# Kernel optimization log

Measured on AMD Instinct MI355X. Metric: run time of the kernel, lower is better.

## Reference

```python
import jax, jax.numpy as jnp
import numpy as np

LAMBDA_SOFTMAX = 9.0
LAMBDA_LSE = 6.0
MARGIN = 0.2
EPS = 1e-8


def setup_inputs() -> dict:
    key = jax.random.key(0)
    k1, k2, k3 = jax.random.split(key, 3)
    Ni, R, W, d = 128, 36, 50, 1024
    im = jax.random.normal(k1, (Ni, R, d), dtype=jnp.float32)
    s = jax.random.normal(k2, (Ni, W, d), dtype=jnp.float32)
    s_l = jax.random.randint(k3, (Ni,), 5, W + 1, dtype=jnp.int32)
    return {"im": im, "s": s, "s_l": s_l}


def _scan_t2i_scores(im, s, s_l):
    # im: (Ni, R, d) images; s: (Nc, W, d) captions; s_l: (Nc,) caption lengths
    Nc, W, _ = s.shape
    word_mask = jnp.arange(W)[None, :] < s_l[:, None]          # (Nc, W)
    # attn[c,i,r,w] = <im[i,r], s[c,w]>  (bmm(context, query^T) per caption)
    attn = jnp.einsum('ird,cwd->cirw', im, s)                  # (Nc, Ni, R, W)
    # clipped_l2norm: LeakyReLU(0.1) then l2-normalize over word dim
    attn = jax.nn.leaky_relu(attn, 0.1)
    attn = attn * word_mask[:, None, None, :]                  # zero padded words
    norm = jnp.sqrt(jnp.sum(attn * attn, axis=3, keepdims=True)) + EPS
    attn = attn / norm
    # transpose to (Nc, Ni, W, R), smooth-softmax over regions
    attn_t = jax.nn.softmax(jnp.swapaxes(attn, 2, 3) * LAMBDA_SOFTMAX, axis=-1)
    # weighted image context per word: (Nc, Ni, W, d)
    wei = jnp.einsum('ird,ciwr->ciwd', im, attn_t)
    # cosine similarity along d between cap word and weighted context
    w12 = jnp.einsum('cwd,ciwd->ciw', s, wei)                  # (Nc, Ni, W)
    w1 = jnp.linalg.norm(s, axis=-1)                           # (Nc, W)
    w2 = jnp.linalg.norm(wei, axis=-1)                         # (Nc, Ni, W)
    row_sim = w12 / jnp.clip(w1[:, None, :] * w2, EPS, None)
    # LogSumExp aggregation over valid words only
    e = jnp.where(word_mask[:, None, :], jnp.exp(row_sim * LAMBDA_LSE), 0.0)
    sims = jnp.log(jnp.sum(e, axis=2)) / LAMBDA_LSE            # (Nc, Ni)
    return sims.T                                              # scores[i, c]


def reference(im, s, s_l) -> jnp.ndarray:
    scores = _scan_t2i_scores(im, s, s_l)                      # (Ni, Nc), Ni == Nc
    diag = jnp.diag(scores)[:, None]
    cost_s = jnp.clip(MARGIN + scores - diag, 0.0, None)       # caption retrieval
    cost_im = jnp.clip(MARGIN + scores - diag.T, 0.0, None)    # image retrieval
    eye = jnp.eye(scores.shape[0], dtype=bool)
    cost_s = jnp.where(eye, 0.0, cost_s)
    cost_im = jnp.where(eye, 0.0, cost_im)
    # max_violation=True: hardest negative per row/column
    return jnp.max(cost_s, axis=1).sum() + jnp.max(cost_im, axis=0).sum()
```

## Files before the change

kernel.cpp:

```cpp
#include <hip/hip_runtime.h>
#include <hip/hip_bf16.h>
#include <cstdint>

using u16 = unsigned short;
using u32 = unsigned int;
using bf16x8 = __attribute__((ext_vector_type(8))) short;
using f32x4  = __attribute__((ext_vector_type(4))) float;

#define NI 128
#define NC 128
#define RR 36
#define WW 50
#define DD 1024
#define LDC 6400
#define ATS 37
#define IMN ((size_t)NI * RR * DD)
#define SN  ((size_t)NC * WW * DD)

#define GLL16(g, l) __builtin_amdgcn_global_load_lds(                        \
    (const __attribute__((address_space(1))) void*)(g),                      \
    (__attribute__((address_space(3))) void*)(l), 16, 0, 0)

typedef const __attribute__((address_space(4))) float cfloat;

__device__ __forceinline__ float2 bf16pair(u32 u) {
  float2 f;
  f.x = __uint_as_float(u << 16);
  f.y = __uint_as_float(u & 0xffff0000u);
  return f;
}

__device__ __forceinline__ u32 bf16_rne(u32 x) {
  return (x + 0x7FFFu + ((x >> 16) & 1u)) >> 16;
}

__global__ __launch_bounds__(256) void detect_dtype(const u16* __restrict__ im,
                                                    int* __restrict__ flag) {
  __shared__ int cnt;
  if (threadIdx.x == 0) cnt = 0;
  __syncthreads();
  int local = 0;
#pragma unroll
  for (int v = 0; v < 32; ++v) {
    u16 u = im[threadIdx.x * 32 + v];
    int e = (u >> 7) & 0xFF;
    if (e >= 0xC0) local++;
  }
  atomicAdd(&cnt, local);
  __syncthreads();
  if (threadIdx.x == 0) *flag = (cnt > 8) ? 1 : 0;
}

__global__ __launch_bounds__(256) void convert_in(const void* __restrict__ im_in,
                                                  const void* __restrict__ s_in,
                                                  u16* __restrict__ imB,
                                                  u16* __restrict__ sB,
                                                  const int* __restrict__ flag) {
  if (*flag == 0) return;
  const size_t TOT8 = (IMN + SN) / 8;
  const size_t stride = (size_t)gridDim.x * blockDim.x;
  for (size_t g = (size_t)blockIdx.x * blockDim.x + threadIdx.x; g < TOT8; g += stride) {
    size_t base = g * 8;
    const u32* sp;
    u16* dst;
    if (base < IMN) { sp = (const u32*)im_in + base; dst = imB + base; }
    else            { sp = (const u32*)s_in + (base - IMN); dst = sB + (base - IMN); }
    u16 o[8];
#pragma unroll
    for (int e = 0; e < 8; ++e) o[e] = (u16)bf16_rne(sp[e]);
    *(uint4*)dst = *(const uint4*)o;
  }
}

__global__ __launch_bounds__(64) void w1_k(const u16* __restrict__ s_orig,
                                           const u16* __restrict__ s_conv,
                                           const int* __restrict__ flag,
                                           float* __restrict__ w1) {
  const u16* s = *flag ? s_conv : s_orig;
  const int cw = blockIdx.x;
  const int lane = threadIdx.x;
  const u16* sp = s + (size_t)cw * DD + lane * 16;
  uint4 A0 = *(const uint4*)sp;
  uint4 A1 = *(const uint4*)(sp + 8);
  float sum = 0.f;
  u32 uu[8] = {A0.x, A0.y, A0.z, A0.w, A1.x, A1.y, A1.z, A1.w};
#pragma unroll
  for (int e = 0; e < 8; ++e) {
    float2 f = bf16pair(uu[e]);
    sum += f.x * f.x + f.y * f.y;
  }
#pragma unroll
  for (int off = 32; off > 0; off >>= 1) sum += __shfl_down(sum, off);
  if (lane == 0) w1[cw] = sqrtf(sum);
}

__global__ __launch_bounds__(256) void gram_k(const u16* __restrict__ im_orig,
                                              const u16* __restrict__ im_conv,
                                              const int* __restrict__ flag,
                                              float* __restrict__ G) {
  const u16* im = *flag ? im_conv : im_orig;
  __shared__ u16 ims[48 * 520];
  const int b = blockIdx.x;
  const int t = threadIdx.x;
  const int lane = t & 63, wv = t >> 6;
  const int lm = lane & 15, q = lane >> 4;
  f32x4 acc[3][3] = {};

  for (int p = 0; p < 2; ++p) {
    const int kk = p * 512;
#pragma unroll
    for (int v = 0; v < 9; ++v) {
      int u = t + v * 256;
      int row = u >> 6;
      int kloc = (u & 63) * 8;
      uint4 val = *(const uint4*)(im + (size_t)b * (RR * DD) + (size_t)row * DD + kk + kloc);
      *(uint4*)&ims[row * 520 + kloc] = val;
    }
    if (p == 0) {
#pragma unroll
      for (int v = 0; v < 4; ++v) {
        int u = t + v * 256;
        if (u < 780) {
          uint4 z; z.x = 0; z.y = 0; z.z = 0; z.w = 0;
          *(uint4*)&ims[36 * 520 + u * 8] = z;
        }
      }
    }
    __syncthreads();
#pragma unroll
    for (int kq = 0; kq < 4; ++kq) {
      const int ks = wv * 4 + kq;
      bf16x8 af[3];
#pragma unroll
      for (int mi = 0; mi < 3; ++mi)
        af[mi] = *(const bf16x8*)&ims[(mi * 16 + lm) * 520 + ks * 32 + q * 8];
#pragma unroll
      for (int mi = 0; mi < 3; ++mi)
#pragma unroll
        for (int ni = 0; ni < 3; ++ni)
          acc[mi][ni] = __builtin_amdgcn_mfma_f32_16x16x32_bf16(af[mi], af[ni], acc[mi][ni], 0, 0, 0);
    }
    __syncthreads();
  }
  float* red = (float*)ims;
  if (wv > 0) {
#pragma unroll
    for (int mi = 0; mi < 3; ++mi)
#pragma unroll
      for (int ni = 0; ni < 3; ++ni)
#pragma unroll
        for (int v = 0; v < 4; ++v) {
          int row = mi * 16 + q * 4 + v;
          int col = ni * 16 + lm;
          red[(wv - 1) * 2304 + row * 48 + col] = acc[mi][ni][v];
        }
  }
  __syncthreads();
  if (wv == 0) {
#pragma unroll
    for (int mi = 0; mi < 3; ++mi)
#pragma unroll
      for (int ni = 0; ni < 3; ++ni)
#pragma unroll
        for (int v = 0; v < 4; ++v) {
          int row = mi * 16 + q * 4 + v;
          int col = ni * 16 + lm;
          float r0 = acc[mi][ni][v] + red[row * 48 + col] +
                     red[2304 + row * 48 + col] + red[4608 + row * 48 + col];
          if (row < RR && col < RR)
            G[(size_t)b * (RR * RR) + row * RR + col] = r0;
        }
  }
}

__global__ __launch_bounds__(256) void gemm_raw(const u16* __restrict__ A_orig,
                                                const u16* __restrict__ A_conv,
                                                const u16* __restrict__ B_orig,
                                                const u16* __restrict__ B_conv,
                                                const int* __restrict__ flag,
                                                u16* __restrict__ C) {
  const u16* A = *flag ? A_conv : A_orig;
  const u16* B = *flag ? B_conv : B_orig;
  __shared__ u16 As[128 * 32];
  __shared__ u16 Bs[128 * 32];
  const int t = threadIdx.x;
  const int col0 = blockIdx.x * 128;
  const int row0 = blockIdx.y * 128;
  const int lane = t & 63, wv = t >> 6;
  const int wm = wv >> 1, wn = wv & 1;
  const int lm = lane & 15, q = lane >> 4;
  f32x4 acc[4][4] = {};

  const int u0 = t, u1 = t + 256;
  const u16* a0 = A + (size_t)(row0 + (u0 >> 2)) * DD + (u0 & 3) * 8;
  const u16* a1 = A + (size_t)(row0 + (u1 >> 2)) * DD + (u1 & 3) * 8;
  const u16* b0 = B + (size_t)(col0 + (u0 >> 2)) * DD + (u0 & 3) * 8;
  const u16* b1 = B + (size_t)(col0 + (u1 >> 2)) * DD + (u1 & 3) * 8;

  for (int k0 = 0; k0 < DD; k0 += 32) {
    GLL16(a0 + k0, &As[u0 * 8]);
    GLL16(a1 + k0, &As[u1 * 8]);
    GLL16(b0 + k0, &Bs[u0 * 8]);
    GLL16(b1 + k0, &Bs[u1 * 8]);
    __syncthreads();
    bf16x8 af[4], bf[4];
#pragma unroll
    for (int mi = 0; mi < 4; ++mi)
      af[mi] = *(const bf16x8*)&As[(wm * 64 + mi * 16 + lm) * 32 + q * 8];
#pragma unroll
    for (int ni = 0; ni < 4; ++ni)
      bf[ni] = *(const bf16x8*)&Bs[(wn * 64 + ni * 16 + lm) * 32 + q * 8];
#pragma unroll
    for (int mi = 0; mi < 4; ++mi)
#pragma unroll
      for (int ni = 0; ni < 4; ++ni)
        acc[mi][ni] = __builtin_amdgcn_mfma_f32_16x16x32_bf16(af[mi], bf[ni], acc[mi][ni], 0, 0, 0);
    __syncthreads();
  }
#pragma unroll
  for (int mi = 0; mi < 4; ++mi)
#pragma unroll
    for (int ni = 0; ni < 4; ++ni)
#pragma unroll
      for (int v = 0; v < 4; ++v) {
        int rr = row0 + wm * 64 + mi * 16 + q * 4 + v;
        int cc = col0 + wn * 64 + ni * 16 + lm;
        C[(size_t)rr * LDC + cc] = (u16)bf16_rne(__float_as_uint(acc[mi][ni][v]));
      }
}

__global__ __launch_bounds__(256, 2) void postproc(const u16* __restrict__ raw,
                                                   const float* __restrict__ G,
                                                   const float* __restrict__ w1,
                                                   const int* __restrict__ s_l,
                                                   float* __restrict__ scores) {
  const int i = blockIdx.y;
  const int wv = threadIdx.x >> 6;
  const int c = blockIdx.x * 4 + wv;
  const int lane = threadIdx.x & 63;
  __shared__ float aT[4][WW * ATS];
  __shared__ float nrm9_s[4][RR];
  const int L = s_l[c];

  if (lane < RR) {
    const u16* rp = raw + (size_t)(i * RR + lane) * LDC + c * WW;
    float sum = 0.f;
#pragma unroll
    for (int j = 0; j < 25; ++j) {
      float2 v = bf16pair(((const u32*)rp)[j]);
      float x0 = v.x > 0.f ? v.x : 0.1f * v.x;
      float x1 = v.y > 0.f ? v.y : 0.1f * v.y;
      if (2 * j     >= L) x0 = 0.f;
      if (2 * j + 1 >= L) x1 = 0.f;
      aT[wv][(2 * j) * ATS + lane]     = x0;
      aT[wv][(2 * j + 1) * ATS + lane] = x1;
      sum += x0 * x0 + x1 * x1;
    }
    nrm9_s[wv][lane] = 9.0f / (sqrtf(sum) + 1e-8f);
  }
  __syncthreads();

  const int wIdx = lane < WW ? lane : WW - 1;
  const float* row = &aT[wv][wIdx * ATS];
  cfloat* Gp = (cfloat*)(G + (size_t)i * (RR * RR));

  float x[RR];
  float m = -1e30f;
#pragma unroll
  for (int r = 0; r < RR; ++r) {
    x[r] = row[r];
    m = fmaxf(m, x[r] * nrm9_s[wv][r]);
  }
  float e[RR];
  float sum = 0.f, w12r = 0.f;
#pragma unroll
  for (int r = 0; r < RR; ++r) {
    float er = __expf(x[r] * nrm9_s[wv][r] - m);
    e[r] = er;
    sum += er;
    w12r += er * (x[r] > 0.f ? x[r] : 10.0f * x[r]);
  }
  float qq2 = 0.f;
#pragma unroll
  for (int r = 0; r < RR; ++r) {
    float h = 0.5f * Gp[r * RR + r] * e[r];
#pragma unroll
    for (int j = r + 1; j < RR; ++j)
      h += Gp[r * RR + j] * e[j];
    qq2 += e[r] * h;
  }
  float qq = 2.0f * qq2;
  float w1v = w1[c * WW + wIdx];
  float denom = fmaxf(w1v * sqrtf(fmaxf(qq, 0.f)), 1e-8f * sum);
  float rs = w12r / denom;
  float ew = (lane < L) ? __expf(6.0f * rs) : 0.f;
#pragma unroll
  for (int off = 32; off > 0; off >>= 1) ew += __shfl_down(ew, off);
  if (lane == 0) scores[i * NC + c] = logf(ew) * (1.0f / 6.0f);
}

__global__ __launch_bounds__(128) void loss_k(const float* __restrict__ scores,
                                              u32* __restrict__ out) {
  __shared__ float diag[NI];
  __shared__ float red[NI];
  const int t = threadIdx.x;
  diag[t] = scores[t * NC + t];
  __syncthreads();
  const float di = diag[t];
  float rowmax = 0.f, colmax = 0.f;
  for (int k = 0; k < NC; ++k) {
    if (k != t) {
      float sr = scores[t * NC + k];
      rowmax = fmaxf(rowmax, fmaxf(0.2f + sr - di, 0.f));
      float sc = scores[k * NC + t];
      colmax = fmaxf(colmax, fmaxf(0.2f + sc - di, 0.f));
    }
  }
  red[t] = rowmax + colmax;
  __syncthreads();
  for (int st = 64; st > 0; st >>= 1) {
    if (t < st) red[t] += red[t + st];
    __syncthreads();
  }
  if (t == 0) {
    u32 b = bf16_rne(__float_as_uint(red[0]));
    out[0] = b | (b << 16);
  }
}

extern "C" void kernel_launch(void* const* d_in, const int* in_sizes, int n_in,
                              void* d_out, int out_size, void* d_ws, size_t ws_size,
                              hipStream_t stream) {
  const void* im_in = d_in[0];
  const void* s_in  = d_in[1];
  const int*  sl    = (const int*)d_in[2];

  char* ws = (char*)d_ws;
  u16*   imB    = (u16*)ws;
  u16*   sB     = (u16*)(ws + 9437184);
  u16*   raw    = (u16*)(ws + 22544384);
  float* G      = (float*)(ws + 22544384 + 58982400);
  float* w1     = G + 128 * RR * RR;
  float* scores = w1 + NC * WW;
  int*   flag   = (int*)(scores + NI * NC);

  detect_dtype<<<dim3(1), dim3(256), 0, stream>>>((const u16*)im_in, flag);
  convert_in<<<dim3(2048), dim3(256), 0, stream>>>(im_in, s_in, imB, sB, flag);
  w1_k<<<dim3(NC * WW), dim3(64), 0, stream>>>((const u16*)s_in, sB, flag, w1);
  gram_k<<<dim3(128), dim3(256), 0, stream>>>((const u16*)im_in, imB, flag, G);
  gemm_raw<<<dim3(50, 36), dim3(256), 0, stream>>>((const u16*)im_in, imB,
                                                   (const u16*)s_in, sB, flag, raw);
  postproc<<<dim3(32, 128), dim3(256), 0, stream>>>(raw, G, w1, sl, scores);
  loss_k<<<dim3(1), dim3(128), 0, stream>>>(scores, (u32*)d_out);
}
```

Before: 285.1 us.

## Fuse dtype detection into conversion, merge w1 into gram, widen GEMM K-tile with swizzle

Dtype detection now runs inside every convert_in block, and the separate detect kernel launch is removed. The caption-norm computation is folded into the Gram kernel so one launch does both. The bf16 GEMM now stages 64-wide K tiles with an XOR-swizzled LDS layout, which halves the barrier count and is meant to reduce bank conflicts. The cost is redundant detection reads in each block, a looser detection threshold over a smaller sample, and more LDS per block.

```diff
diff --git a/kernel.cpp b/kernel.cpp
--- a/kernel.cpp
+++ b/kernel.cpp
@@ -34,29 +34,27 @@
   return (x + 0x7FFFu + ((x >> 16) & 1u)) >> 16;
 }
 
-__global__ __launch_bounds__(256) void detect_dtype(const u16* __restrict__ im,
-                                                    int* __restrict__ flag) {
-  __shared__ int cnt;
-  if (threadIdx.x == 0) cnt = 0;
-  __syncthreads();
-  int local = 0;
-#pragma unroll
-  for (int v = 0; v < 32; ++v) {
-    u16 u = im[threadIdx.x * 32 + v];
-    int e = (u >> 7) & 0xFF;
-    if (e >= 0xC0) local++;
-  }
-  atomicAdd(&cnt, local);
-  __syncthreads();
-  if (threadIdx.x == 0) *flag = (cnt > 8) ? 1 : 0;
-}
-
 __global__ __launch_bounds__(256) void convert_in(const void* __restrict__ im_in,
                                                   const void* __restrict__ s_in,
                                                   u16* __restrict__ imB,
                                                   u16* __restrict__ sB,
-                                                  const int* __restrict__ flag) {
-  if (*flag == 0) return;
+                                                  int* __restrict__ flag) {
+  __shared__ int cnt;
+  if (threadIdx.x == 0) cnt = 0;
+  __syncthreads();
+  const u16* imu = (const u16*)im_in;
+  int local = 0;
+#pragma unroll
+  for (int v = 0; v < 16; ++v) {
+    u16 u = imu[threadIdx.x * 16 + v];
+    if (((u >> 7) & 0xFF) >= 0xC0) local++;
+  }
+  if (local) atomicAdd(&cnt, local);
+  __syncthreads();
+  const int f = (cnt > 4) ? 1 : 0;
+  if (blockIdx.x == 0 && threadIdx.x == 0) *flag = f;
+  if (!f) return;
+
   const size_t TOT8 = (IMN + SN) / 8;
   const size_t stride = (size_t)gridDim.x * blockDim.x;
   for (size_t g = (size_t)blockIdx.x * blockDim.x + threadIdx.x; g < TOT8; g += stride) {
@@ -72,33 +70,15 @@
   }
 }
 
-__global__ __launch_bounds__(64) void w1_k(const u16* __restrict__ s_orig,
-                                           const u16* __restrict__ s_conv,
-                                           const int* __restrict__ flag,
-                                           float* __restrict__ w1) {
-  const u16* s = *flag ? s_conv : s_orig;
-  const int cw = blockIdx.x;
-  const int lane = threadIdx.x;
-  const u16* sp = s + (size_t)cw * DD + lane * 16;
-  uint4 A0 = *(const uint4*)sp;
-  uint4 A1 = *(const uint4*)(sp + 8);
-  float sum = 0.f;
-  u32 uu[8] = {A0.x, A0.y, A0.z, A0.w, A1.x, A1.y, A1.z, A1.w};
-#pragma unroll
-  for (int e = 0; e < 8; ++e) {
-    float2 f = bf16pair(uu[e]);
-    sum += f.x * f.x + f.y * f.y;
-  }
-#pragma unroll
-  for (int off = 32; off > 0; off >>= 1) sum += __shfl_down(sum, off);
-  if (lane == 0) w1[cw] = sqrtf(sum);
-}
-
-__global__ __launch_bounds__(256) void gram_k(const u16* __restrict__ im_orig,
-                                              const u16* __restrict__ im_conv,
-                                              const int* __restrict__ flag,
-                                              float* __restrict__ G) {
+__global__ __launch_bounds__(256) void gram_w1(const u16* __restrict__ im_orig,
+                                               const u16* __restrict__ im_conv,
+                                               const u16* __restrict__ s_orig,
+                                               const u16* __restrict__ s_conv,
+                                               const int* __restrict__ flag,
+                                               float* __restrict__ G,
+                                               float* __restrict__ w1) {
   const u16* im = *flag ? im_conv : im_orig;
+  const u16* s  = *flag ? s_conv : s_orig;
   __shared__ u16 ims[48 * 520];
   const int b = blockIdx.x;
   const int t = threadIdx.x;
@@ -171,6 +151,22 @@
             G[(size_t)b * (RR * RR) + row * RR + col] = r0;
         }
   }
+  const u16* sc = s + (size_t)b * WW * DD;
+  for (int w = wv; w < WW; w += 4) {
+    const u16* sp = sc + (size_t)w * DD + lane * 16;
+    uint4 A0 = *(const uint4*)sp;
+    uint4 A1 = *(const uint4*)(sp + 8);
+    float sum = 0.f;
+    u32 uu[8] = {A0.x, A0.y, A0.z, A0.w, A1.x, A1.y, A1.z, A1.w};
+#pragma unroll
+    for (int e = 0; e < 8; ++e) {
+      float2 f = bf16pair(uu[e]);
+      sum += f.x * f.x + f.y * f.y;
+    }
+#pragma unroll
+    for (int off = 32; off > 0; off >>= 1) sum += __shfl_down(sum, off);
+    if (lane == 0) w1[b * WW + w] = sqrtf(sum);
+  }
 }
 
 __global__ __launch_bounds__(256) void gemm_raw(const u16* __restrict__ A_orig,
@@ -181,8 +177,8 @@
                                                 u16* __restrict__ C) {
   const u16* A = *flag ? A_conv : A_orig;
   const u16* B = *flag ? B_conv : B_orig;
-  __shared__ u16 As[128 * 32];
-  __shared__ u16 Bs[128 * 32];
+  __shared__ u16 As[128 * 64];
+  __shared__ u16 Bs[128 * 64];
   const int t = threadIdx.x;
   const int col0 = blockIdx.x * 128;
   const int row0 = blockIdx.y * 128;
@@ -191,30 +187,39 @@
   const int lm = lane & 15, q = lane >> 4;
   f32x4 acc[4][4] = {};
 
-  const int u0 = t, u1 = t + 256;
-  const u16* a0 = A + (size_t)(row0 + (u0 >> 2)) * DD + (u0 & 3) * 8;
-  const u16* a1 = A + (size_t)(row0 + (u1 >> 2)) * DD + (u1 & 3) * 8;
-  const u16* b0 = B + (size_t)(col0 + (u0 >> 2)) * DD + (u0 & 3) * 8;
-  const u16* b1 = B + (size_t)(col0 + (u1 >> 2)) * DD + (u1 & 3) * 8;
-
-  for (int k0 = 0; k0 < DD; k0 += 32) {
-    GLL16(a0 + k0, &As[u0 * 8]);
-    GLL16(a1 + k0, &As[u1 * 8]);
-    GLL16(b0 + k0, &Bs[u0 * 8]);
-    GLL16(b1 + k0, &Bs[u1 * 8]);
-    __syncthreads();
-    bf16x8 af[4], bf[4];
-#pragma unroll
-    for (int mi = 0; mi < 4; ++mi)
-      af[mi] = *(const bf16x8*)&As[(wm * 64 + mi * 16 + lm) * 32 + q * 8];
-#pragma unroll
-    for (int ni = 0; ni < 4; ++ni)
-      bf[ni] = *(const bf16x8*)&Bs[(wn * 64 + ni * 16 + lm) * 32 + q * 8];
-#pragma unroll
-    for (int mi = 0; mi < 4; ++mi)
+  const u16* ap[4];
+  const u16* bp[4];
+#pragma unroll
+  for (int v = 0; v < 4; ++v) {
+    int u = t + v * 256;
+    int row = u >> 3;
+    int c = (u & 7) ^ (row & 7);
+    ap[v] = A + (size_t)(row0 + row) * DD + c * 8;
+    bp[v] = B + (size_t)(col0 + row) * DD + c * 8;
+  }
+
+  for (int k0 = 0; k0 < DD; k0 += 64) {
+#pragma unroll
+    for (int v = 0; v < 4; ++v) GLL16(ap[v] + k0, &As[(t + v * 256) * 8]);
+#pragma unroll
+    for (int v = 0; v < 4; ++v) GLL16(bp[v] + k0, &Bs[(t + v * 256) * 8]);
+    __syncthreads();
+#pragma unroll
+    for (int ks = 0; ks < 2; ++ks) {
+      bf16x8 af[4], bf[4];
+      const int pch = (ks * 4 + q) ^ (lm & 7);
+#pragma unroll
+      for (int mi = 0; mi < 4; ++mi)
+        af[mi] = *(const bf16x8*)&As[(wm * 64 + mi * 16 + lm) * 64 + pch * 8];
 #pragma unroll
       for (int ni = 0; ni < 4; ++ni)
-        acc[mi][ni] = __builtin_amdgcn_mfma_f32_16x16x32_bf16(af[mi], bf[ni], acc[mi][ni], 0, 0, 0);
+        bf[ni] = *(const bf16x8*)&Bs[(wn * 64 + ni * 16 + lm) * 64 + pch * 8];
+#pragma unroll
+      for (int mi = 0; mi < 4; ++mi)
+#pragma unroll
+        for (int ni = 0; ni < 4; ++ni)
+          acc[mi][ni] = __builtin_amdgcn_mfma_f32_16x16x32_bf16(af[mi], bf[ni], acc[mi][ni], 0, 0, 0);
+    }
     __syncthreads();
   }
 #pragma unroll
@@ -344,10 +349,9 @@
   float* scores = w1 + NC * WW;
   int*   flag   = (int*)(scores + NI * NC);
 
-  detect_dtype<<<dim3(1), dim3(256), 0, stream>>>((const u16*)im_in, flag);
   convert_in<<<dim3(2048), dim3(256), 0, stream>>>(im_in, s_in, imB, sB, flag);
-  w1_k<<<dim3(NC * WW), dim3(64), 0, stream>>>((const u16*)s_in, sB, flag, w1);
-  gram_k<<<dim3(128), dim3(256), 0, stream>>>((const u16*)im_in, imB, flag, G);
+  gram_w1<<<dim3(128), dim3(256), 0, stream>>>((const u16*)im_in, imB,
+                                               (const u16*)s_in, sB, flag, G, w1);
   gemm_raw<<<dim3(50, 36), dim3(256), 0, stream>>>((const u16*)im_in, imB,
                                                    (const u16*)s_in, sB, flag, raw);
   postproc<<<dim3(32, 128), dim3(256), 0, stream>>>(raw, G, w1, sl, scores);
```

Result: faster. 277.3 us (-2.7%).
